# Kernel optimization log

Measured on AMD Instinct MI355X. Metric: run time of the kernel, lower is better.

The kernel has to match this reference:

```python
import jax, jax.numpy as jnp
import numpy as np

N_R = 256          # number of relations
N_HOP_MAX = 3      # max hops
N_E = 200_000      # number of entities
N_T = 1_000_000    # number of KB triples
B = 32             # batch size
D_Q = 768          # BERT question embedding dim
D_IN = D_Q + (N_HOP_MAX - 1) * N_R  # input width of dense_inf / dense_att


def setup_inputs() -> dict:
    key = jax.random.key(0)
    ks = jax.random.split(key, 7)
    x = (jax.random.uniform(ks[0], (B, N_E)) < 0.001).astype(jnp.float32)
    h_q = jax.random.normal(ks[1], (B, D_Q), jnp.float32)
    W_inf = jax.random.normal(ks[2], (N_R, D_IN), jnp.float32) * 0.02
    W_att = jax.random.normal(ks[3], (1, D_IN), jnp.float32) * 0.02
    subj_idx = jax.random.randint(ks[4], (N_T,), 0, N_E, jnp.int32)
    rel_idx = jax.random.randint(ks[5], (N_T,), 0, N_R, jnp.int32)
    obj_idx = jax.random.randint(ks[6], (N_T,), 0, N_E, jnp.int32)
    return {"x": x, "h_q": h_q, "W_inf": W_inf, "W_att": W_att,
            "subj_idx": subj_idx, "rel_idx": rel_idx, "obj_idx": obj_idx,
            "n_hop": N_HOP_MAX}


def _one_step(x, r, subj_idx, rel_idx, obj_idx):
    # Equivalent to ((x @ M_subj.T) * (r @ M_rel.T)) @ M_obj with 0/1
    # indicator matrices: gather - elementwise multiply - scatter-add.
    x_t = jnp.take(x, subj_idx, axis=1)   # (B, N_T)
    r_t = jnp.take(r, rel_idx, axis=1)    # (B, N_T)
    prod = x_t * r_t                       # (B, N_T)
    # scatter-add over triples into object entities: (N_T, B) -> (N_E, B)
    return jax.ops.segment_sum(prod.T, obj_idx, num_segments=x.shape[1]).T


def reference(x, h_q, W_inf, W_att, subj_idx, rel_idx, obj_idx, n_hop):
    rs, cs, xs = [], [], []
    for i in range(n_hop):
        if i:
            # most-recent relation first, then older ones (rs[::-1])
            concat = jnp.concatenate([h_q] + rs[::-1], axis=1)
        else:
            concat = h_q
        pad = jnp.zeros((h_q.shape[0], (N_HOP_MAX - 1 - i) * N_R), h_q.dtype)
        concat = jnp.concatenate([concat, pad], axis=1)  # (B, D_IN)
        r = concat @ W_inf.T   # (B, N_R)
        c = concat @ W_att.T   # (B, 1)
        x = _one_step(x, r, subj_idx, rel_idx, obj_idx)  # (B, N_E)
        rs.append(r)
        cs.append(c)
        xs.append(x)
    a = jax.nn.softmax(jnp.concatenate(cs, axis=1), axis=-1)  # (B, n_hop)
    y = jnp.einsum('bh,bhe->be', a, jnp.stack(xs, axis=1))     # (B, N_E)
    return y
```

## Files before the change

kernel.cpp:

```cpp
#include <hip/hip_runtime.h>

#define N_R   256
#define N_E   200000
#define N_T   1000000
#define B     32
#define D_Q   768
#define D_IN  1280

__global__ void k_mask0(const float* __restrict__ x, unsigned* __restrict__ mask0) {
    int e = blockIdx.x * 256 + threadIdx.x;
    if (e >= N_E) return;
    unsigned m = 0;
#pragma unroll 8
    for (int b = 0; b < 32; ++b)
        m |= (x[(size_t)b * N_E + e] != 0.f ? 1u : 0u) << b;
    mask0[e] = m;
}

__global__ void k_r0(const float* __restrict__ h_q, const float* __restrict__ W_inf,
                     float* __restrict__ rT0) {
    __shared__ float hs[32 * 257];
    __shared__ float red[256];
    int t = threadIdx.x, rel = blockIdx.x;
    int b = t & 31, kp = t >> 5;
    float acc = 0.f;
    for (int c = 0; c < 3; ++c) {
        __syncthreads();
#pragma unroll
        for (int i = 0; i < 32; ++i)
            hs[i * 257 + t] = h_q[i * D_Q + c * 256 + t];
        __syncthreads();
        const float* w = &W_inf[rel * D_IN + c * 256 + kp * 32];
#pragma unroll
        for (int i = 0; i < 32; ++i)
            acc += w[i] * hs[b * 257 + kp * 32 + i];
    }
    red[t] = acc;
    __syncthreads();
    if (t < 32) {
        float s = 0.f;
        for (int q = 0; q < 8; ++q) s += red[q * 32 + t];
        rT0[rel * 32 + t] = s;
    }
}

__global__ void k_r12(const float* __restrict__ W_inf, const float* __restrict__ rT0,
                      const float* __restrict__ rPrev, float* __restrict__ rOut,
                      int hop2) {
    __shared__ float red[256];
    int t = threadIdx.x, rel = blockIdx.x;
    int b = t & 31, jp = t >> 5;
    const float* w2 = &W_inf[rel * D_IN + D_Q];
    float acc = 0.f;
#pragma unroll 8
    for (int jj = 0; jj < 32; ++jj) {
        int j = jp * 32 + jj;
        acc += w2[j] * rPrev[j * 32 + b];
    }
    if (hop2) {
        const float* w3 = w2 + N_R;
#pragma unroll 8
        for (int jj = 0; jj < 32; ++jj) {
            int j = jp * 32 + jj;
            acc += w3[j] * rT0[j * 32 + b];
        }
    }
    red[t] = acc;
    __syncthreads();
    if (t < 32) {
        float s = rT0[rel * 32 + t];
        for (int q = 0; q < 8; ++q) s += red[q * 32 + t];
        rOut[rel * 32 + t] = s;
    }
}

__global__ void k_att(const float* __restrict__ h_q, const float* __restrict__ W_att,
                      const float* __restrict__ rT0, const float* __restrict__ rT1,
                      float* __restrict__ a_w) {
    __shared__ float p0[256], p1[256], p2[256], p3[256];
    int t = threadIdx.x;
    int b = t & 31, p = t >> 5;
    float c0 = 0.f;
    for (int k = p * 96; k < p * 96 + 96; ++k) c0 += W_att[k] * h_q[b * D_Q + k];
    float s1 = 0.f, s2 = 0.f, s3 = 0.f;
    for (int j = p * 32; j < p * 32 + 32; ++j) {
        float w2 = W_att[D_Q + j], w3 = W_att[D_Q + N_R + j];
        float r0v = rT0[j * 32 + b], r1v = rT1[j * 32 + b];
        s1 += w2 * r0v; s2 += w2 * r1v; s3 += w3 * r0v;
    }
    p0[t] = c0; p1[t] = s1; p2[t] = s2; p3[t] = s3;
    __syncthreads();
    if (t < 32) {
        float C0 = 0.f, S1 = 0.f, S2 = 0.f, S3 = 0.f;
        for (int q = 0; q < 8; ++q) {
            C0 += p0[q * 32 + t]; S1 += p1[q * 32 + t];
            S2 += p2[q * 32 + t]; S3 += p3[q * 32 + t];
        }
        float c1 = C0 + S1, c2 = C0 + S2 + S3;
        float m  = fmaxf(C0, fmaxf(c1, c2));
        float e0 = __expf(C0 - m), e1 = __expf(c1 - m), e2 = __expf(c2 - m);
        float inv = 1.f / (e0 + e1 + e2);
        a_w[t] = e0 * inv; a_w[32 + t] = e1 * inv; a_w[64 + t] = e2 * inv;
    }
}

template <bool BN_LAYOUT, bool HAS_NEXT>
__global__ void k_hop(const float* __restrict__ xIn,
                      const unsigned* __restrict__ maskIn,
                      const float* __restrict__ rT, const float* __restrict__ aw,
                      const int* __restrict__ subj, const int* __restrict__ rel,
                      const int* __restrict__ obj,
                      float* __restrict__ xOut, unsigned* __restrict__ maskOut,
                      float* __restrict__ outp) {
    int i = blockIdx.x * 256 + threadIdx.x;
    if (i >= N_T) return;
    int s = subj[i];
    unsigned m = maskIn[s];
    if (!m) return;
    int r = rel[i];
    int o = obj[i];
    const float* rrow = rT + r * 32;
    unsigned mm = m;
    while (mm) {
        int b = __ffs(mm) - 1;
        mm &= mm - 1;
        float v = BN_LAYOUT ? xIn[(size_t)b * N_E + s] : xIn[s * 32 + b];
        float c = v * rrow[b];
        if (HAS_NEXT) unsafeAtomicAdd(&xOut[o * 32 + b], c);
        unsafeAtomicAdd(&outp[(size_t)b * N_E + o], aw[b] * c);
    }
    if (HAS_NEXT) atomicOr(&maskOut[o], m);
}

extern "C" void kernel_launch(void* const* d_in, const int* in_sizes, int n_in,
                              void* d_out, int out_size, void* d_ws, size_t ws_size,
                              hipStream_t stream) {
    const float* x     = (const float*)d_in[0];
    const float* h_q   = (const float*)d_in[1];
    const float* W_inf = (const float*)d_in[2];
    const float* W_att = (const float*)d_in[3];
    const int*   subj  = (const int*)d_in[4];
    const int*   rel   = (const int*)d_in[5];
    const int*   obj   = (const int*)d_in[6];
    float* out = (float*)d_out;

    const size_t NEB = (size_t)N_E * B;
    float*    bufA  = (float*)d_ws;
    float*    bufB  = bufA + NEB;
    float*    rT    = bufB + NEB;
    float*    a_w   = rT + 3 * N_R * B;
    unsigned* mask1 = (unsigned*)(a_w + 96);
    unsigned* mask2 = mask1 + N_E;
    unsigned* mask0 = mask2 + N_E;

    const int EB  = (N_E + 255) / 256;
    const int TBL = (N_T + 255) / 256;

    hipMemsetAsync(bufA, 0, 2 * NEB * sizeof(float), stream);
    hipMemsetAsync(mask1, 0, 2 * N_E * sizeof(unsigned), stream);
    hipMemsetAsync(out, 0, NEB * sizeof(float), stream);

    k_mask0<<<EB, 256, 0, stream>>>(x, mask0);

    k_r0 <<<N_R, 256, 0, stream>>>(h_q, W_inf, rT);
    k_r12<<<N_R, 256, 0, stream>>>(W_inf, rT, rT, rT + N_R * B, 0);
    k_r12<<<N_R, 256, 0, stream>>>(W_inf, rT, rT + N_R * B, rT + 2 * N_R * B, 1);
    k_att<<<1, 256, 0, stream>>>(h_q, W_att, rT, rT + N_R * B, a_w);

    k_hop<true, true><<<TBL, 256, 0, stream>>>(x, mask0, rT, a_w,
                                               subj, rel, obj, bufA, mask1, out);
    k_hop<false, true><<<TBL, 256, 0, stream>>>(bufA, mask1, rT + N_R * B, a_w + 32,
                                                subj, rel, obj, bufB, mask2, out);
    k_hop<false, false><<<TBL, 256, 0, stream>>>(bufB, mask2, rT + 2 * N_R * B, a_w + 64,
                                                 subj, rel, obj, (float*)0,
                                                 (unsigned*)0, out);
}
```

Measured before the change: 215.9 us.

## Fuse zeroing into mask prep, vectorize triple loads, fold final attention weight

The three memset calls and the mask kernel become one prep kernel that zeroes the ping-pong buffers, the output and the masks with float4 stores while building the seed mask. The hop kernel now handles four triples per thread, loading subject, relation and object indices as int4. The last hop's attention weight is folded into the third relation vector, so that hop needs only one atomic per contribution. This cuts launch count and per-thread index overhead, but gives fewer threads per hop and more per-thread divergence.

```diff
diff --git a/kernel.cpp b/kernel.cpp
--- a/kernel.cpp
+++ b/kernel.cpp
@@ -7,14 +7,27 @@
 #define D_Q   768
 #define D_IN  1280
 
-__global__ void k_mask0(const float* __restrict__ x, unsigned* __restrict__ mask0) {
-    int e = blockIdx.x * 256 + threadIdx.x;
-    if (e >= N_E) return;
-    unsigned m = 0;
+__global__ void k_prep(const float* __restrict__ x, unsigned* __restrict__ mask0,
+                       unsigned* __restrict__ mask1, unsigned* __restrict__ mask2,
+                       float4* __restrict__ bufs ,
+                       float4* __restrict__ outv) {
+    int tid = blockIdx.x * 256 + threadIdx.x;
+    float4 z = {0.f, 0.f, 0.f, 0.f};
+#pragma unroll
+    for (int i = 0; i < 4; ++i)
+        bufs[(size_t)i * 800000 + tid] = z;
+#pragma unroll
+    for (int i = 0; i < 2; ++i)
+        outv[(size_t)i * 800000 + tid] = z;
+    if (tid < N_E) {
+        unsigned m = 0;
 #pragma unroll 8
-    for (int b = 0; b < 32; ++b)
-        m |= (x[(size_t)b * N_E + e] != 0.f ? 1u : 0u) << b;
-    mask0[e] = m;
+        for (int b = 0; b < 32; ++b)
+            m |= (x[(size_t)b * N_E + tid] != 0.f ? 1u : 0u) << b;
+        mask0[tid] = m;
+        mask1[tid] = 0u;
+        mask2[tid] = 0u;
+    }
 }
 
 __global__ void k_r0(const float* __restrict__ h_q, const float* __restrict__ W_inf,
@@ -46,7 +59,7 @@
 
 __global__ void k_r12(const float* __restrict__ W_inf, const float* __restrict__ rT0,
                       const float* __restrict__ rPrev, float* __restrict__ rOut,
-                      int hop2) {
+                      int hop2, const float* __restrict__ a_scale) {
     __shared__ float red[256];
     int t = threadIdx.x, rel = blockIdx.x;
     int b = t & 31, jp = t >> 5;
@@ -70,6 +83,7 @@
     if (t < 32) {
         float s = rT0[rel * 32 + t];
         for (int q = 0; q < 8; ++q) s += red[q * 32 + t];
+        if (a_scale) s *= a_scale[t];
         rOut[rel * 32 + t] = s;
     }
 }
@@ -108,28 +122,42 @@
 __global__ void k_hop(const float* __restrict__ xIn,
                       const unsigned* __restrict__ maskIn,
                       const float* __restrict__ rT, const float* __restrict__ aw,
-                      const int* __restrict__ subj, const int* __restrict__ rel,
-                      const int* __restrict__ obj,
+                      const int4* __restrict__ subj4, const int4* __restrict__ rel4,
+                      const int4* __restrict__ obj4,
                       float* __restrict__ xOut, unsigned* __restrict__ maskOut,
                       float* __restrict__ outp) {
-    int i = blockIdx.x * 256 + threadIdx.x;
-    if (i >= N_T) return;
-    int s = subj[i];
-    unsigned m = maskIn[s];
-    if (!m) return;
-    int r = rel[i];
-    int o = obj[i];
-    const float* rrow = rT + r * 32;
-    unsigned mm = m;
-    while (mm) {
-        int b = __ffs(mm) - 1;
-        mm &= mm - 1;
-        float v = BN_LAYOUT ? xIn[(size_t)b * N_E + s] : xIn[s * 32 + b];
-        float c = v * rrow[b];
-        if (HAS_NEXT) unsafeAtomicAdd(&xOut[o * 32 + b], c);
-        unsafeAtomicAdd(&outp[(size_t)b * N_E + o], aw[b] * c);
-    }
-    if (HAS_NEXT) atomicOr(&maskOut[o], m);
+    int tid = blockIdx.x * 256 + threadIdx.x;
+    if (tid >= N_T / 4) return;
+    int4 s4 = subj4[tid];
+    unsigned m0 = maskIn[s4.x], m1 = maskIn[s4.y];
+    unsigned m2 = maskIn[s4.z], m3 = maskIn[s4.w];
+    if (!(m0 | m1 | m2 | m3)) return;
+    int4 r4 = rel4[tid];
+    int4 o4 = obj4[tid];
+    int      ss[4] = {s4.x, s4.y, s4.z, s4.w};
+    unsigned mk[4] = {m0, m1, m2, m3};
+    int      rr[4] = {r4.x, r4.y, r4.z, r4.w};
+    int      oo[4] = {o4.x, o4.y, o4.z, o4.w};
+#pragma unroll
+    for (int k = 0; k < 4; ++k) {
+        unsigned mm = mk[k];
+        if (!mm) continue;
+        int s = ss[k], o = oo[k];
+        const float* rrow = rT + rr[k] * 32;
+        while (mm) {
+            int b = __ffs(mm) - 1;
+            mm &= mm - 1;
+            float v = BN_LAYOUT ? xIn[(size_t)b * N_E + s] : xIn[s * 32 + b];
+            float c = v * rrow[b];
+            if (HAS_NEXT) {
+                unsafeAtomicAdd(&xOut[o * 32 + b], c);
+                unsafeAtomicAdd(&outp[(size_t)b * N_E + o], aw[b] * c);
+            } else {
+                unsafeAtomicAdd(&outp[(size_t)b * N_E + o], c);
+            }
+        }
+        if (HAS_NEXT) atomicOr(&maskOut[o], mk[k]);
+    }
 }
 
 extern "C" void kernel_launch(void* const* d_in, const int* in_sizes, int n_in,
@@ -149,29 +177,31 @@
     float*    bufB  = bufA + NEB;
     float*    rT    = bufB + NEB;
     float*    a_w   = rT + 3 * N_R * B;
-    unsigned* mask1 = (unsigned*)(a_w + 96);
+    unsigned* mask0 = (unsigned*)(a_w + 96);
+    unsigned* mask1 = mask0 + N_E;
     unsigned* mask2 = mask1 + N_E;
-    unsigned* mask0 = mask2 + N_E;
-
-    const int EB  = (N_E + 255) / 256;
-    const int TBL = (N_T + 255) / 256;
-
-    hipMemsetAsync(bufA, 0, 2 * NEB * sizeof(float), stream);
-    hipMemsetAsync(mask1, 0, 2 * N_E * sizeof(unsigned), stream);
-    hipMemsetAsync(out, 0, NEB * sizeof(float), stream);
-
-    k_mask0<<<EB, 256, 0, stream>>>(x, mask0);
+
+    const int PB  = 3125;
+    const int HB  = (N_T / 4 + 255) / 256;
+
+    k_prep<<<PB, 256, 0, stream>>>(x, mask0, mask1, mask2,
+                                   (float4*)bufA, (float4*)out);
 
     k_r0 <<<N_R, 256, 0, stream>>>(h_q, W_inf, rT);
-    k_r12<<<N_R, 256, 0, stream>>>(W_inf, rT, rT, rT + N_R * B, 0);
-    k_r12<<<N_R, 256, 0, stream>>>(W_inf, rT, rT + N_R * B, rT + 2 * N_R * B, 1);
+    k_r12<<<N_R, 256, 0, stream>>>(W_inf, rT, rT, rT + N_R * B, 0, (const float*)0);
     k_att<<<1, 256, 0, stream>>>(h_q, W_att, rT, rT + N_R * B, a_w);
-
-    k_hop<true, true><<<TBL, 256, 0, stream>>>(x, mask0, rT, a_w,
-                                               subj, rel, obj, bufA, mask1, out);
-    k_hop<false, true><<<TBL, 256, 0, stream>>>(bufA, mask1, rT + N_R * B, a_w + 32,
-                                                subj, rel, obj, bufB, mask2, out);
-    k_hop<false, false><<<TBL, 256, 0, stream>>>(bufB, mask2, rT + 2 * N_R * B, a_w + 64,
-                                                 subj, rel, obj, (float*)0,
-                                                 (unsigned*)0, out);
-}
+    k_r12<<<N_R, 256, 0, stream>>>(W_inf, rT, rT + N_R * B, rT + 2 * N_R * B, 1,
+                                   a_w + 64);
+
+    k_hop<true, true><<<HB, 256, 0, stream>>>(x, mask0, rT, a_w,
+                                              (const int4*)subj, (const int4*)rel,
+                                              (const int4*)obj, bufA, mask1, out);
+    k_hop<false, true><<<HB, 256, 0, stream>>>(bufA, mask1, rT + N_R * B, a_w + 32,
+                                               (const int4*)subj, (const int4*)rel,
+                                               (const int4*)obj, bufB, mask2, out);
+    k_hop<false, false><<<HB, 256, 0, stream>>>(bufB, mask2, rT + 2 * N_R * B,
+                                                (const float*)0,
+                                                (const int4*)subj, (const int4*)rel,
+                                                (const int4*)obj, (float*)0,
+                                                (unsigned*)0, out);
+}
```

New measurement: 219.9 us. Within noise of the previous version (+1.8%).
